# Kernel optimization log

Measured on AMD Instinct MI355X. Metric: run time of the kernel, lower is better.

## Reference

```python
import jax, jax.numpy as jnp
import numpy as np

GROUP_SIZE = 128


def setup_inputs() -> dict:
    key = jax.random.key(0)
    k1, k2, k3 = jax.random.split(key, 3)
    x = (jax.random.normal(k1, (4, 2048, 4096), dtype=jnp.float32)).astype(jnp.float16)
    packed_weight = jax.random.randint(k2, (512, 11008), 0, 2147483647, dtype=jnp.int32)
    scales = jax.random.uniform(k3, (32, 11008), dtype=jnp.float32).astype(jnp.float16)
    return {"x": x, "packed_weight": packed_weight, "scales": scales}


def _dequantize(packed_weight, scales):
    # packed_weight: [K//8, N] int32, 8 nibbles per int32 (nibble i at bits 4i..4i+3)
    # scales: [K//GROUP_SIZE, N]
    Kp, N = packed_weight.shape
    K = Kp * 8
    shifts = (jnp.arange(8, dtype=jnp.int32) * 4)[None, :, None]      # [1,8,1]
    nibbles = (packed_weight[:, None, :] >> shifts) & 15              # [K//8,8,N]
    vals = nibbles.reshape(K, N).astype(jnp.float32)                  # [K,N]
    sc = jnp.repeat(scales.astype(jnp.float32), GROUP_SIZE, axis=0)   # [K,N]
    return (vals - 8.0) / 7.5 * sc


def reference(x, packed_weight, scales):
    K = packed_weight.shape[0] * 8
    N = packed_weight.shape[1]
    deq = _dequantize(packed_weight, scales)                 # [K,N] fp32
    x2 = x.reshape(-1, K).astype(jnp.float32)                # [M,K] fp32 accumulate
    out = jnp.matmul(x2, deq).astype(jnp.float16)            # [M,N] fp16 store
    return out.reshape(*x.shape[:-1], N)
```

## Files before the change

### kernel.cpp

```cpp
#include <hip/hip_runtime.h>
#include <stdint.h>

typedef __attribute__((ext_vector_type(8))) _Float16 half8;
typedef __attribute__((ext_vector_type(2))) _Float16 half2v;
typedef __attribute__((ext_vector_type(4))) float floatx4;
typedef __attribute__((ext_vector_type(4))) uint32_t uint4v;

#define KDIM 4096
#define NDIM 11008
#define NKT 64

#define GLOAD_LDS16(gsrc, ldst)                                                        \
  __builtin_amdgcn_global_load_lds(                                                    \
      (const __attribute__((address_space(1))) void*)(gsrc),                           \
      (__attribute__((address_space(3))) void*)(ldst), 16, 0, 0)

static __device__ __forceinline__ uint32_t pkrtz(float a, float b) {
  auto h = __builtin_amdgcn_cvt_pkrtz(a, b);
  return __builtin_bit_cast(uint32_t, h);
}

static __device__ __forceinline__ half8 dq8(uint32_t q, half2v ssv) {
  half2v off; off[0] = (_Float16)(-1032.0f); off[1] = (_Float16)(-1032.0f);
  const uint32_t a0 = (q & 0x000F000Fu) | 0x64006400u;
  const uint32_t a1 = ((q >> 4) & 0x000F000Fu) | 0x64006400u;
  const uint32_t a2 = ((q >> 8) & 0x000F000Fu) | 0x64006400u;
  const uint32_t a3 = ((q >> 12) & 0x000F000Fu) | 0x64006400u;
  const uint32_t p0 = __builtin_amdgcn_perm(a1, a0, 0x05040100u);
  const uint32_t p1 = __builtin_amdgcn_perm(a3, a2, 0x05040100u);
  const uint32_t p2 = __builtin_amdgcn_perm(a1, a0, 0x07060302u);
  const uint32_t p3 = __builtin_amdgcn_perm(a3, a2, 0x07060302u);
  uint4v u;
  u[0] = __builtin_bit_cast(uint32_t, (__builtin_bit_cast(half2v, p0) + off) * ssv);
  u[1] = __builtin_bit_cast(uint32_t, (__builtin_bit_cast(half2v, p1) + off) * ssv);
  u[2] = __builtin_bit_cast(uint32_t, (__builtin_bit_cast(half2v, p2) + off) * ssv);
  u[3] = __builtin_bit_cast(uint32_t, (__builtin_bit_cast(half2v, p3) + off) * ssv);
  return __builtin_bit_cast(half8, u);
}

__global__ __launch_bounds__(256)
void l4b_prep(const float* __restrict__ in, _Float16* __restrict__ out, int n8) {
  int i = blockIdx.x * 256 + threadIdx.x;
  if (i < n8) {
    floatx4 v0 = ((const floatx4*)in)[2 * i];
    floatx4 v1 = ((const floatx4*)in)[2 * i + 1];
    uint4v u;
    u[0] = pkrtz(v0[0], v0[1]); u[1] = pkrtz(v0[2], v0[3]);
    u[2] = pkrtz(v1[0], v1[1]); u[3] = pkrtz(v1[2], v1[3]);
    ((uint4v*)out)[i] = u;
  }
}

__global__ __launch_bounds__(512, 2)
void l4b_main(const _Float16* __restrict__ XH,
              const int* __restrict__ PW,
              const float* __restrict__ SC,
              float* __restrict__ OUT)
{
  __shared__ alignas(16) _Float16 la[2][256 * 64];
  __shared__ alignas(16) _Float16 lb[2][256 * 64];

  const int tid  = threadIdx.x;
  const int lane = tid & 63;
  const int wave = tid >> 6;

  const int cpx = (int)gridDim.x >> 3;
  const int wg  = ((int)blockIdx.x & 7) * cpx + ((int)blockIdx.x >> 3);
  const int by  = wg / 43;
  const int bx  = wg - by * 43;
  const int64_t brow = (int64_t)by * 256;
  const int     bcol = bx * 256;

  const int wr = (wave >> 2) * 128;
  const int wc = (wave & 3) * 64;
  const int fr = lane & 15;
  const int fq = lane >> 4;

  floatx4 acc[8][4];
#pragma unroll
  for (int i = 0; i < 8; ++i)
#pragma unroll
    for (int j = 0; j < 4; ++j) acc[i][j] = (floatx4)(0.0f);

  const int arow8 = lane >> 3;
  const int aslot = (lane & 7) ^ arow8;
  const _Float16* const asrc0 =
      XH + (brow + wave * 32 + arow8) * (int64_t)KDIM + aslot * 8;

  const int bc  = tid & 255;
  const int bkq = tid >> 8;
  const int*   const pwcol = PW + bcol + bc;
  const float* const sccol = SC + bcol + bc;

  int   rw[4];
  float rsc;

#define DMA_A(t, b)                                                        \
  do {                                                                     \
    _Pragma("unroll") for (int g8 = 0; g8 < 4; ++g8)                       \
        GLOAD_LDS16(asrc0 + (int64_t)g8 * 8 * KDIM + (t) * 64,             \
                    &la[b][(wave * 32 + g8 * 8) * 64]);                    \
  } while (0)

#define LOADB(t)                                                           \
  do {                                                                     \
    const int* pp = pwcol + ((t) * 8 + bkq) * NDIM;                        \
    _Pragma("unroll") for (int j_ = 0; j_ < 4; ++j_)                       \
        rw[j_] = pp[j_ * 2 * NDIM];                                        \
    rsc = sccol[(int64_t)((t) >> 1) * NDIM];                               \
  } while (0)

#define WRITE_B(dst)                                                       \
  do {                                                                     \
    const _Float16 ss = (_Float16)(rsc * (1.0f / 7.5f));                   \
    half2v sv; sv[0] = ss; sv[1] = ss;                                     \
    _Pragma("unroll") for (int j_ = 0; j_ < 4; ++j_) {                     \
      half8 v = dq8((uint32_t)rw[j_], sv);                                 \
      const int kp = bkq + 2 * j_;                                         \
      *(half8*)&(dst)[bc * 64 + ((kp ^ (bc & 7)) * 8)] = v;                \
    }                                                                      \
  } while (0)

#define READ_B4(ksl)                                                       \
  _Pragma("unroll") for (int fn_ = 0; fn_ < 4; ++fn_) {                    \
    const int n_ = wc + fn_ * 16 + fr;                                     \
    bfr[fn_] = *(const half8*)&lbp[n_ * 64 + (((ksl) ^ (n_ & 7)) * 8)];    \
  }

#define READ_A4(fm0, ksl)                                                  \
  _Pragma("unroll") for (int fm_ = 0; fm_ < 4; ++fm_) {                    \
    const int m_ = wr + ((fm0) + fm_) * 16 + fr;                           \
    af[fm_] = *(const half8*)&lap[m_ * 64 + (((ksl) ^ (m_ & 7)) * 8)];     \
  }

#define MFMA16(fm0)                                                        \
  __builtin_amdgcn_s_setprio(1);                                           \
  _Pragma("unroll") for (int fm_ = 0; fm_ < 4; ++fm_)                      \
  _Pragma("unroll") for (int fn_ = 0; fn_ < 4; ++fn_)                      \
      acc[(fm0) + fm_][fn_] = __builtin_amdgcn_mfma_f32_16x16x32_f16(      \
          af[fm_], bfr[fn_], acc[(fm0) + fm_][fn_], 0, 0, 0);              \
  __builtin_amdgcn_s_setprio(0);

#define PH_BAR()                                                           \
  do {                                                                     \
    __builtin_amdgcn_sched_barrier(0);                                     \
    __builtin_amdgcn_s_barrier();                                          \
    __builtin_amdgcn_sched_barrier(0);                                     \
  } while (0)

  LOADB(0);
  DMA_A(0, 0);
  WRITE_B(lb[0]);
  __builtin_amdgcn_sched_barrier(0);
  asm volatile("s_waitcnt vmcnt(0) lgkmcnt(0)" ::: "memory");
  __builtin_amdgcn_s_barrier();
  __builtin_amdgcn_sched_barrier(0);

  for (int kt = 0; kt < NKT; ++kt) {
    const int buf = kt & 1;
    const _Float16* lap = la[buf];
    const _Float16* lbp = lb[buf];
    _Float16* const lbn = lb[buf ^ 1];
    const bool havep = (kt + 1 < NKT);

    half8 af[4], bfr[4];

    READ_B4(fq);
    READ_A4(0, fq);
    if (havep) {
      LOADB(kt + 1);
      DMA_A(kt + 1, buf ^ 1);
    }
    PH_BAR();
    MFMA16(0);
    PH_BAR();

    READ_A4(4, fq);
    PH_BAR();
    MFMA16(4);
    PH_BAR();

    READ_B4(4 + fq);
    READ_A4(0, 4 + fq);
    if (havep) WRITE_B(lbn);
    PH_BAR();
    MFMA16(0);
    PH_BAR();

    READ_A4(4, 4 + fq);
    PH_BAR();
    MFMA16(4);
    __builtin_amdgcn_sched_barrier(0);
    asm volatile("s_waitcnt vmcnt(0) lgkmcnt(0)" ::: "memory");
    __builtin_amdgcn_s_barrier();
    __builtin_amdgcn_sched_barrier(0);
  }

#pragma unroll
  for (int fm = 0; fm < 8; ++fm)
#pragma unroll
    for (int fn = 0; fn < 4; ++fn)
#pragma unroll
      for (int r = 0; r < 4; ++r) {
        const int64_t row = brow + wr + fm * 16 + fq * 4 + r;
        const int     col = bcol + wc + fn * 16 + fr;
        OUT[row * NDIM + col] = acc[fm][fn][r];
      }
}

__global__ __launch_bounds__(512, 2)
void l4b_fb(const float* __restrict__ X, const int* __restrict__ PW,
            const float* __restrict__ SC, float* __restrict__ OUT)
{
  __shared__ alignas(16) _Float16 fla[2][256 * 64];
  __shared__ alignas(16) _Float16 flb[2][256 * 64];

  const int tid  = threadIdx.x;
  const int lane = tid & 63;
  const int wave = tid >> 6;

  const int cpx = (int)gridDim.x >> 3;
  const int wg  = ((int)blockIdx.x & 7) * cpx + ((int)blockIdx.x >> 3);
  const int by  = wg / 43;
  const int bx  = wg - by * 43;
  const int64_t brow = (int64_t)by * 256;
  const int     bcol = bx * 256;

  const int wr = (wave >> 2) * 128;
  const int wc = (wave & 3) * 64;
  const int fr = lane & 15;
  const int fq = lane >> 4;

  floatx4 acc[8][4];
#pragma unroll
  for (int i = 0; i < 8; ++i)
#pragma unroll
    for (int j = 0; j < 4; ++j) acc[i][j] = (floatx4)(0.0f);

  const int ar = tid >> 1;
  const int ah = tid & 1;
  const float* const aptr = X + (brow + ar) * (int64_t)KDIM + ah * 32;
  const int bc  = tid & 255;
  const int bkq = tid >> 8;
  const int*   const pwcol = PW + bcol + bc;
  const float* const sccol = SC + bcol + bc;

  floatx4 ra[8];
  int     rwf[4];
  float   rsc;

#define F_LOAD_A(t)                                                        \
  do {                                                                     \
    const float* ap = aptr + (t) * 64;                                     \
    _Pragma("unroll") for (int i_ = 0; i_ < 8; ++i_)                       \
        ra[i_] = *(const floatx4*)(ap + i_ * 4);                           \
  } while (0)

#define F_LOAD_B(t)                                                        \
  do {                                                                     \
    const int* pp = pwcol + ((t) * 8 + bkq) * NDIM;                        \
    _Pragma("unroll") for (int j_ = 0; j_ < 4; ++j_)                       \
        rwf[j_] = pp[j_ * 2 * NDIM];                                       \
    rsc = sccol[(int64_t)((t) >> 1) * NDIM];                               \
  } while (0)

#define F_WRITE_A(dst)                                                     \
  do {                                                                     \
    _Pragma("unroll") for (int i2 = 0; i2 < 4; ++i2) {                     \
      uint4v u;                                                            \
      u[0] = pkrtz(ra[2 * i2][0], ra[2 * i2][1]);                          \
      u[1] = pkrtz(ra[2 * i2][2], ra[2 * i2][3]);                          \
      u[2] = pkrtz(ra[2 * i2 + 1][0], ra[2 * i2 + 1][1]);                  \
      u[3] = pkrtz(ra[2 * i2 + 1][2], ra[2 * i2 + 1][3]);                  \
      const int s_ = ah * 4 + i2;                                          \
      *(half8*)&(dst)[ar * 64 + ((s_ ^ (ar & 7)) * 8)] =                   \
          __builtin_bit_cast(half8, u);                                    \
    }                                                                      \
  } while (0)

#define F_WRITE_B(dst)                                                     \
  do {                                                                     \
    const _Float16 ssf = (_Float16)(rsc * (1.0f / 7.5f));                  \
    half2v sv; sv[0] = ssf; sv[1] = ssf;                                   \
    _Pragma("unroll") for (int j_ = 0; j_ < 4; ++j_) {                     \
      half8 v = dq8((uint32_t)rwf[j_], sv);                                \
      const int kp = bkq + 2 * j_;                                         \
      *(half8*)&(dst)[bc * 64 + ((kp ^ (bc & 7)) * 8)] = v;                \
    }                                                                      \
  } while (0)

#define F_MFMA16(fm0)                                                      \
  __builtin_amdgcn_s_barrier();                                            \
  asm volatile("s_waitcnt lgkmcnt(0)" ::: "memory");                       \
  __builtin_amdgcn_sched_barrier(0);                                       \
  __builtin_amdgcn_s_setprio(1);                                           \
  _Pragma("unroll") for (int fm_ = 0; fm_ < 4; ++fm_)                      \
  _Pragma("unroll") for (int fn_ = 0; fn_ < 4; ++fn_)                      \
      acc[(fm0) + fm_][fn_] = __builtin_amdgcn_mfma_f32_16x16x32_f16(      \
          af[fm_], bfr[fn_], acc[(fm0) + fm_][fn_], 0, 0, 0);              \
  __builtin_amdgcn_s_setprio(0);                                           \
  __builtin_amdgcn_sched_barrier(0);                                       \
  __builtin_amdgcn_s_barrier();                                            \
  __builtin_amdgcn_sched_barrier(0);

  F_LOAD_A(0); F_LOAD_B(0);
  F_WRITE_A(fla[0]); F_WRITE_B(flb[0]);
  F_LOAD_A(1); F_LOAD_B(1);
  asm volatile("s_waitcnt lgkmcnt(0)" ::: "memory");
  __builtin_amdgcn_s_barrier();
  __builtin_amdgcn_sched_barrier(0);

  for (int kt = 0; kt < NKT; ++kt) {
    const int buf = kt & 1;
    const _Float16* lap = fla[buf];
    const _Float16* lbp = flb[buf];
    _Float16* const lan = fla[buf ^ 1];
    _Float16* const lbn = flb[buf ^ 1];
    const bool haveW = (kt + 1 < NKT);
    const bool haveL = (kt + 2 < NKT);

    half8 bfr[4], af[4];

#pragma unroll
    for (int fn_ = 0; fn_ < 4; ++fn_) {
      const int n_ = wc + fn_ * 16 + fr;
      bfr[fn_] = *(const half8*)&lbp[n_ * 64 + ((fq ^ (n_ & 7)) * 8)];
    }
#pragma unroll
    for (int fm_ = 0; fm_ < 4; ++fm_) {
      const int m_ = wr + fm_ * 16 + fr;
      af[fm_] = *(const half8*)&lap[m_ * 64 + ((fq ^ (m_ & 7)) * 8)];
    }
    if (haveW) F_WRITE_A(lan);
    F_MFMA16(0);

#pragma unroll
    for (int fm_ = 0; fm_ < 4; ++fm_) {
      const int m_ = wr + (4 + fm_) * 16 + fr;
      af[fm_] = *(const half8*)&lap[m_ * 64 + ((fq ^ (m_ & 7)) * 8)];
    }
    if (haveL) F_LOAD_A(kt + 2);
    F_MFMA16(4);

#pragma unroll
    for (int fn_ = 0; fn_ < 4; ++fn_) {
      const int n_ = wc + fn_ * 16 + fr;
      bfr[fn_] = *(const half8*)&lbp[n_ * 64 + (((4 + fq) ^ (n_ & 7)) * 8)];
    }
#pragma unroll
    for (int fm_ = 0; fm_ < 4; ++fm_) {
      const int m_ = wr + fm_ * 16 + fr;
      af[fm_] = *(const half8*)&lap[m_ * 64 + (((4 + fq) ^ (m_ & 7)) * 8)];
    }
    if (haveW) F_WRITE_B(lbn);
    F_MFMA16(0);

#pragma unroll
    for (int fm_ = 0; fm_ < 4; ++fm_) {
      const int m_ = wr + (4 + fm_) * 16 + fr;
      af[fm_] = *(const half8*)&lap[m_ * 64 + (((4 + fq) ^ (m_ & 7)) * 8)];
    }
    if (haveL) F_LOAD_B(kt + 2);
    F_MFMA16(4);
  }

#pragma unroll
  for (int fm = 0; fm < 8; ++fm)
#pragma unroll
    for (int fn = 0; fn < 4; ++fn)
#pragma unroll
      for (int r = 0; r < 4; ++r) {
        const int64_t row = brow + wr + fm * 16 + fq * 4 + r;
        const int     col = bcol + wc + fn * 16 + fr;
        OUT[row * NDIM + col] = acc[fm][fn][r];
      }
}

extern "C" void kernel_launch(void* const* d_in, const int* in_sizes, int n_in,
                              void* d_out, int out_size, void* d_ws, size_t ws_size,
                              hipStream_t stream) {
  const float* X   = (const float*)d_in[0];
  const int*   PW  = (const int*)d_in[1];
  const float* SC  = (const float*)d_in[2];
  float*       OUT = (float*)d_out;

  const int    M     = in_sizes[0] / KDIM;
  const size_t needH = (size_t)in_sizes[0] * 2;
  const int    grid  = (M / 256) * (NDIM / 256);

  if (ws_size >= needH && (M % 256) == 0) {
    _Float16* XH = (_Float16*)d_ws;
    const int n8 = in_sizes[0] / 8;
    l4b_prep<<<(n8 + 255) / 256, 256, 0, stream>>>(X, XH, n8);
    l4b_main<<<grid, 512, 0, stream>>>(XH, PW, SC, OUT);
  } else {
    l4b_fb<<<grid, 512, 0, stream>>>(X, PW, SC, OUT);
  }
}
```

Measured before the change: 850.3 us.

## Deepen global-load pipeline to prefetch two k-tiles ahead with register double-buffering

Restructures the main loop so global loads for A (DMA into LDS) and packed B weights are issued two k-tiles ahead instead of one. B weights go into alternating register sets, and A reuses the just-consumed LDS buffer. It uses partial vmcnt waits so the next tile's loads stay in flight across the barrier. This is meant to hide more global memory latency behind MFMA work, at the cost of extra registers and trickier synchronization.

After: 858.5 us. No clear change (+1.0%).

```diff
diff --git a/kernel.cpp b/kernel.cpp
--- a/kernel.cpp
+++ b/kernel.cpp
@@ -92,45 +92,45 @@
   const int*   const pwcol = PW + bcol + bc;
   const float* const sccol = SC + bcol + bc;
 
-  int   rw[4];
-  float rsc;
-
-#define DMA_A(t, b)                                                        \
+  int   rw0[4], rw1[4];
+  float rs0, rs1;
+
+#define DMA_A(t, dst)                                                      \
   do {                                                                     \
     _Pragma("unroll") for (int g8 = 0; g8 < 4; ++g8)                       \
         GLOAD_LDS16(asrc0 + (int64_t)g8 * 8 * KDIM + (t) * 64,             \
-                    &la[b][(wave * 32 + g8 * 8) * 64]);                    \
-  } while (0)
-
-#define LOADB(t)                                                           \
+                    &(dst)[(wave * 32 + g8 * 8) * 64]);                    \
+  } while (0)
+
+#define LOADB(t, rwv, rs)                                                  \
   do {                                                                     \
     const int* pp = pwcol + ((t) * 8 + bkq) * NDIM;                        \
     _Pragma("unroll") for (int j_ = 0; j_ < 4; ++j_)                       \
-        rw[j_] = pp[j_ * 2 * NDIM];                                        \
-    rsc = sccol[(int64_t)((t) >> 1) * NDIM];                               \
-  } while (0)
-
-#define WRITE_B(dst)                                                       \
-  do {                                                                     \
-    const _Float16 ss = (_Float16)(rsc * (1.0f / 7.5f));                   \
+        rwv[j_] = pp[j_ * 2 * NDIM];                                       \
+    rs = sccol[(int64_t)((t) >> 1) * NDIM];                                \
+  } while (0)
+
+#define WRITE_B(dst, rwv, rs)                                              \
+  do {                                                                     \
+    const _Float16 ss = (_Float16)((rs) * (1.0f / 7.5f));                  \
     half2v sv; sv[0] = ss; sv[1] = ss;                                     \
     _Pragma("unroll") for (int j_ = 0; j_ < 4; ++j_) {                     \
-      half8 v = dq8((uint32_t)rw[j_], sv);                                 \
+      half8 v = dq8((uint32_t)rwv[j_], sv);                                \
       const int kp = bkq + 2 * j_;                                         \
       *(half8*)&(dst)[bc * 64 + ((kp ^ (bc & 7)) * 8)] = v;                \
     }                                                                      \
   } while (0)
 
-#define READ_B4(ksl)                                                       \
+#define READ_B4(src, ksl)                                                  \
   _Pragma("unroll") for (int fn_ = 0; fn_ < 4; ++fn_) {                    \
     const int n_ = wc + fn_ * 16 + fr;                                     \
-    bfr[fn_] = *(const half8*)&lbp[n_ * 64 + (((ksl) ^ (n_ & 7)) * 8)];    \
-  }
-
-#define READ_A4(fm0, ksl)                                                  \
+    bfr[fn_] = *(const half8*)&(src)[n_ * 64 + (((ksl) ^ (n_ & 7)) * 8)];  \
+  }
+
+#define READ_A4(src, fm0, ksl)                                             \
   _Pragma("unroll") for (int fm_ = 0; fm_ < 4; ++fm_) {                    \
     const int m_ = wr + ((fm0) + fm_) * 16 + fr;                           \
-    af[fm_] = *(const half8*)&lap[m_ * 64 + (((ksl) ^ (m_ & 7)) * 8)];     \
+    af[fm_] = *(const half8*)&(src)[m_ * 64 + (((ksl) ^ (m_ & 7)) * 8)];   \
   }
 
 #define MFMA16(fm0)                                                        \
@@ -148,53 +148,64 @@
     __builtin_amdgcn_sched_barrier(0);                                     \
   } while (0)
 
-  LOADB(0);
-  DMA_A(0, 0);
-  WRITE_B(lb[0]);
-  __builtin_amdgcn_sched_barrier(0);
-  asm volatile("s_waitcnt vmcnt(0) lgkmcnt(0)" ::: "memory");
+#define KT_BODY(laP, lbP, lbN, rwc, rsc, rwn, rsn, KT, STG, LDF)           \
+  do {                                                                     \
+    half8 af[4], bfr[4];                                                   \
+                                                                   \
+    READ_B4(lbP, fq);                                                      \
+    READ_A4(laP, 0, fq);                                                   \
+    PH_BAR();                                                              \
+    MFMA16(0);                                                             \
+    PH_BAR();                                                              \
+                                                                   \
+    READ_A4(laP, 4, fq);                                                   \
+    PH_BAR();                                                              \
+    MFMA16(4);                                                             \
+    PH_BAR();                                                              \
+                                                \
+    READ_B4(lbP, 4 + fq);                                                  \
+    READ_A4(laP, 0, 4 + fq);                                               \
+    if (STG) WRITE_B(lbN, rwc, rsc);                                       \
+    PH_BAR();                                                              \
+    MFMA16(0);                                                             \
+    PH_BAR();                                                              \
+        \
+    READ_A4(laP, 4, 4 + fq);                                               \
+    asm volatile("s_waitcnt lgkmcnt(0)" ::: "memory");                     \
+    __builtin_amdgcn_sched_barrier(0);                                     \
+    __builtin_amdgcn_s_barrier();        \
+    __builtin_amdgcn_sched_barrier(0);                                     \
+    if (LDF) {                                                             \
+      LOADB(KT + 2, rwn, rsn);                                 \
+      DMA_A(KT + 2, laP);                                      \
+    }                                                                      \
+    __builtin_amdgcn_sched_barrier(0);                                     \
+    MFMA16(4);                                                             \
+    __builtin_amdgcn_sched_barrier(0);                                     \
+    if (LDF) { asm volatile("s_waitcnt vmcnt(9)" ::: "memory"); }          \
+    else     { asm volatile("s_waitcnt vmcnt(0)" ::: "memory"); }          \
+    __builtin_amdgcn_sched_barrier(0);                                     \
+    __builtin_amdgcn_s_barrier();          \
+    __builtin_amdgcn_sched_barrier(0);                                     \
+  } while (0)
+
+  LOADB(0, rw0, rs0);
+  DMA_A(0, la[0]);
+  WRITE_B(lb[0], rw0, rs0);
+  LOADB(1, rw1, rs1);
+  DMA_A(1, la[1]);
+  asm volatile("s_waitcnt vmcnt(9)" ::: "memory");
+  asm volatile("s_waitcnt lgkmcnt(0)" ::: "memory");
   __builtin_amdgcn_s_barrier();
   __builtin_amdgcn_sched_barrier(0);
 
-  for (int kt = 0; kt < NKT; ++kt) {
-    const int buf = kt & 1;
-    const _Float16* lap = la[buf];
-    const _Float16* lbp = lb[buf];
-    _Float16* const lbn = lb[buf ^ 1];
-    const bool havep = (kt + 1 < NKT);
-
-    half8 af[4], bfr[4];
-
-    READ_B4(fq);
-    READ_A4(0, fq);
-    if (havep) {
-      LOADB(kt + 1);
-      DMA_A(kt + 1, buf ^ 1);
-    }
-    PH_BAR();
-    MFMA16(0);
-    PH_BAR();
-
-    READ_A4(4, fq);
-    PH_BAR();
-    MFMA16(4);
-    PH_BAR();
-
-    READ_B4(4 + fq);
-    READ_A4(0, 4 + fq);
-    if (havep) WRITE_B(lbn);
-    PH_BAR();
-    MFMA16(0);
-    PH_BAR();
-
-    READ_A4(4, 4 + fq);
-    PH_BAR();
-    MFMA16(4);
-    __builtin_amdgcn_sched_barrier(0);
-    asm volatile("s_waitcnt vmcnt(0) lgkmcnt(0)" ::: "memory");
-    __builtin_amdgcn_s_barrier();
-    __builtin_amdgcn_sched_barrier(0);
-  }
+  for (int g = 0; g < 31; ++g) {
+    const int kt = 2 * g;
+    KT_BODY(la[0], lb[0], lb[1], rw1, rs1, rw0, rs0, kt,     true, true);
+    KT_BODY(la[1], lb[1], lb[0], rw0, rs0, rw1, rs1, kt + 1, true, true);
+  }
+  KT_BODY(la[0], lb[0], lb[1], rw1, rs1, rw0, rs0, 62, true,  false);
+  KT_BODY(la[1], lb[1], lb[0], rw0, rs0, rw1, rs1, 63, false, false);
 
 #pragma unroll
   for (int fm = 0; fm < 8; ++fm)
```

## Replace 256x256 tile kernel with 128x128 tile, 256-thread kernel with simpler pipeline

Applied to the files above, without the earlier changes.

The main int4-dequant GEMM kernel moves from 256x256 output tiles with 8 waves to 128x128 tiles with 4 waves, each wave still owning a 64x64 sub-tile. The phased barrier schedule with interleaved LDS reads is replaced by a single phase per k-tile: prefetch, read all fragments, run the MFMAs, then dequantize and write the next B tile. The smaller tiles give more workgroups, but each one reuses loaded data less, so global traffic and B dequantization work rise.

After: 982.9 us. 15.6% more time.

```diff
diff --git a/kernel.cpp b/kernel.cpp
--- a/kernel.cpp
+++ b/kernel.cpp
@@ -51,14 +51,14 @@
   }
 }
 
-__global__ __launch_bounds__(512, 2)
-void l4b_main(const _Float16* __restrict__ XH,
+__global__ __launch_bounds__(256, 2)
+void l4b_g128(const _Float16* __restrict__ XH,
               const int* __restrict__ PW,
               const float* __restrict__ SC,
               float* __restrict__ OUT)
 {
-  __shared__ alignas(16) _Float16 la[2][256 * 64];
-  __shared__ alignas(16) _Float16 lb[2][256 * 64];
+  __shared__ alignas(16) _Float16 la[2][128 * 64];
+  __shared__ alignas(16) _Float16 lb[2][128 * 64];
 
   const int tid  = threadIdx.x;
   const int lane = tid & 63;
@@ -66,19 +66,19 @@
 
   const int cpx = (int)gridDim.x >> 3;
   const int wg  = ((int)blockIdx.x & 7) * cpx + ((int)blockIdx.x >> 3);
-  const int by  = wg / 43;
-  const int bx  = wg - by * 43;
-  const int64_t brow = (int64_t)by * 256;
-  const int     bcol = bx * 256;
-
-  const int wr = (wave >> 2) * 128;
-  const int wc = (wave & 3) * 64;
+  const int by  = wg / 86;
+  const int bx  = wg - by * 86;
+  const int64_t brow = (int64_t)by * 128;
+  const int     bcol = bx * 128;
+
+  const int wr = (wave >> 1) * 64;
+  const int wc = (wave & 1) * 64;
   const int fr = lane & 15;
   const int fq = lane >> 4;
 
-  floatx4 acc[8][4];
-#pragma unroll
-  for (int i = 0; i < 8; ++i)
+  floatx4 acc[4][4];
+#pragma unroll
+  for (int i = 0; i < 4; ++i)
 #pragma unroll
     for (int j = 0; j < 4; ++j) acc[i][j] = (floatx4)(0.0f);
 
@@ -87,32 +87,32 @@
   const _Float16* const asrc0 =
       XH + (brow + wave * 32 + arow8) * (int64_t)KDIM + aslot * 8;
 
-  const int bc  = tid & 255;
-  const int bkq = tid >> 8;
+  const int bc  = tid & 127;
+  const int bkq = tid >> 7;
   const int*   const pwcol = PW + bcol + bc;
   const float* const sccol = SC + bcol + bc;
 
   int   rw[4];
-  float rsc;
-
-#define DMA_A(t, b)                                                        \
+  float rs;
+
+#define G_DMA_A(t, dst)                                                    \
   do {                                                                     \
     _Pragma("unroll") for (int g8 = 0; g8 < 4; ++g8)                       \
         GLOAD_LDS16(asrc0 + (int64_t)g8 * 8 * KDIM + (t) * 64,             \
-                    &la[b][(wave * 32 + g8 * 8) * 64]);                    \
-  } while (0)
-
-#define LOADB(t)                                                           \
+                    &(dst)[(wave * 32 + g8 * 8) * 64]);                    \
+  } while (0)
+
+#define G_LOADB(t)                                                         \
   do {                                                                     \
     const int* pp = pwcol + ((t) * 8 + bkq) * NDIM;                        \
     _Pragma("unroll") for (int j_ = 0; j_ < 4; ++j_)                       \
         rw[j_] = pp[j_ * 2 * NDIM];                                        \
-    rsc = sccol[(int64_t)((t) >> 1) * NDIM];                               \
-  } while (0)
-
-#define WRITE_B(dst)                                                       \
-  do {                                                                     \
-    const _Float16 ss = (_Float16)(rsc * (1.0f / 7.5f));                   \
+    rs = sccol[(int64_t)((t) >> 1) * NDIM];                                \
+  } while (0)
+
+#define G_WRITE_B(dst)                                                     \
+  do {                                                                     \
+    const _Float16 ss = (_Float16)(rs * (1.0f / 7.5f));                    \
     half2v sv; sv[0] = ss; sv[1] = ss;                                     \
     _Pragma("unroll") for (int j_ = 0; j_ < 4; ++j_) {                     \
       half8 v = dq8((uint32_t)rw[j_], sv);                                 \
@@ -121,75 +121,59 @@
     }                                                                      \
   } while (0)
 
-#define READ_B4(ksl)                                                       \
+#define G_READ_A(dstf, ks)                                                 \
+  _Pragma("unroll") for (int fm_ = 0; fm_ < 4; ++fm_) {                    \
+    const int m_ = wr + fm_ * 16 + fr;                                     \
+    dstf[fm_] = *(const half8*)&lap[m_ * 64 + ((((ks)*4 + fq) ^ (m_ & 7)) * 8)]; \
+  }
+
+#define G_READ_B(dstf, ks)                                                 \
   _Pragma("unroll") for (int fn_ = 0; fn_ < 4; ++fn_) {                    \
     const int n_ = wc + fn_ * 16 + fr;                                     \
-    bfr[fn_] = *(const half8*)&lbp[n_ * 64 + (((ksl) ^ (n_ & 7)) * 8)];    \
-  }
-
-#define READ_A4(fm0, ksl)                                                  \
-  _Pragma("unroll") for (int fm_ = 0; fm_ < 4; ++fm_) {                    \
-    const int m_ = wr + ((fm0) + fm_) * 16 + fr;                           \
-    af[fm_] = *(const half8*)&lap[m_ * 64 + (((ksl) ^ (m_ & 7)) * 8)];     \
-  }
-
-#define MFMA16(fm0)                                                        \
-  __builtin_amdgcn_s_setprio(1);                                           \
-  _Pragma("unroll") for (int fm_ = 0; fm_ < 4; ++fm_)                      \
-  _Pragma("unroll") for (int fn_ = 0; fn_ < 4; ++fn_)                      \
-      acc[(fm0) + fm_][fn_] = __builtin_amdgcn_mfma_f32_16x16x32_f16(      \
-          af[fm_], bfr[fn_], acc[(fm0) + fm_][fn_], 0, 0, 0);              \
-  __builtin_amdgcn_s_setprio(0);
-
-#define PH_BAR()                                                           \
-  do {                                                                     \
-    __builtin_amdgcn_sched_barrier(0);                                     \
-    __builtin_amdgcn_s_barrier();                                          \
-    __builtin_amdgcn_sched_barrier(0);                                     \
-  } while (0)
-
-  LOADB(0);
-  DMA_A(0, 0);
-  WRITE_B(lb[0]);
-  __builtin_amdgcn_sched_barrier(0);
+    dstf[fn_] = *(const half8*)&lbp[n_ * 64 + ((((ks)*4 + fq) ^ (n_ & 7)) * 8)]; \
+  }
+
+  G_LOADB(0);
+  G_DMA_A(0, la[0]);
+  G_WRITE_B(lb[0]);
   asm volatile("s_waitcnt vmcnt(0) lgkmcnt(0)" ::: "memory");
   __builtin_amdgcn_s_barrier();
   __builtin_amdgcn_sched_barrier(0);
 
   for (int kt = 0; kt < NKT; ++kt) {
-    const int buf = kt & 1;
-    const _Float16* lap = la[buf];
-    const _Float16* lbp = lb[buf];
-    _Float16* const lbn = lb[buf ^ 1];
+    const _Float16* lap = la[kt & 1];
+    const _Float16* lbp = lb[kt & 1];
+    _Float16* const lan = la[(kt & 1) ^ 1];
+    _Float16* const lbn = lb[(kt & 1) ^ 1];
     const bool havep = (kt + 1 < NKT);
 
-    half8 af[4], bfr[4];
-
-    READ_B4(fq);
-    READ_A4(0, fq);
     if (havep) {
-      LOADB(kt + 1);
-      DMA_A(kt + 1, buf ^ 1);
-    }
-    PH_BAR();
-    MFMA16(0);
-    PH_BAR();
-
-    READ_A4(4, fq);
-    PH_BAR();
-    MFMA16(4);
-    PH_BAR();
-
-    READ_B4(4 + fq);
-    READ_A4(0, 4 + fq);
-    if (havep) WRITE_B(lbn);
-    PH_BAR();
-    MFMA16(0);
-    PH_BAR();
-
-    READ_A4(4, 4 + fq);
-    PH_BAR();
-    MFMA16(4);
+      G_LOADB(kt + 1);
+      G_DMA_A(kt + 1, lan);
+    }
+    __builtin_amdgcn_sched_barrier(0);
+
+    half8 af0[4], bf0[4], af1[4], bf1[4];
+    G_READ_A(af0, 0); G_READ_B(bf0, 0);
+    G_READ_A(af1, 1); G_READ_B(bf1, 1);
+
+    __builtin_amdgcn_s_setprio(1);
+#pragma unroll
+    for (int fm_ = 0; fm_ < 4; ++fm_)
+#pragma unroll
+      for (int fn_ = 0; fn_ < 4; ++fn_)
+        acc[fm_][fn_] = __builtin_amdgcn_mfma_f32_16x16x32_f16(
+            af0[fm_], bf0[fn_], acc[fm_][fn_], 0, 0, 0);
+#pragma unroll
+    for (int fm_ = 0; fm_ < 4; ++fm_)
+#pragma unroll
+      for (int fn_ = 0; fn_ < 4; ++fn_)
+        acc[fm_][fn_] = __builtin_amdgcn_mfma_f32_16x16x32_f16(
+            af1[fm_], bf1[fn_], acc[fm_][fn_], 0, 0, 0);
+    __builtin_amdgcn_s_setprio(0);
+
+    if (havep) G_WRITE_B(lbn);
+
     __builtin_amdgcn_sched_barrier(0);
     asm volatile("s_waitcnt vmcnt(0) lgkmcnt(0)" ::: "memory");
     __builtin_amdgcn_s_barrier();
@@ -197,7 +181,7 @@
   }
 
 #pragma unroll
-  for (int fm = 0; fm < 8; ++fm)
+  for (int fm = 0; fm < 4; ++fm)
 #pragma unroll
     for (int fn = 0; fn < 4; ++fn)
 #pragma unroll
@@ -386,14 +370,15 @@
 
   const int    M     = in_sizes[0] / KDIM;
   const size_t needH = (size_t)in_sizes[0] * 2;
-  const int    grid  = (M / 256) * (NDIM / 256);
-
-  if (ws_size >= needH && (M % 256) == 0) {
+
+  if (ws_size >= needH && (M % 128) == 0) {
     _Float16* XH = (_Float16*)d_ws;
     const int n8 = in_sizes[0] / 8;
     l4b_prep<<<(n8 + 255) / 256, 256, 0, stream>>>(X, XH, n8);
-    l4b_main<<<grid, 512, 0, stream>>>(XH, PW, SC, OUT);
+    const int grid = (M / 128) * (NDIM / 128);
+    l4b_g128<<<grid, 256, 0, stream>>>(XH, PW, SC, OUT);
   } else {
+    const int grid = (M / 256) * (NDIM / 256);
     l4b_fb<<<grid, 512, 0, stream>>>(X, PW, SC, OUT);
   }
 }
```

## Pre-dequantize weights to fp16 transposed buffer and DMA both operands to LDS

Applied to the files above, without the earlier changes.

Adds a prep kernel that dequantizes the packed int4 weights once per call into an fp16 [N,K] workspace buffer. The GEMM then loads both A and B straight into LDS with global_load_lds, removing per-tile register dequantization and the VALU work inside the main loop. The cost is an extra ~90MB write and read of fp16 weights per call. The existing main kernel's barrier placement is also reshuffled. The new path runs only when the workspace is large enough.

Measured after the change: 872.1 us. +2.6%, slower.

```diff
diff --git a/kernel.cpp b/kernel.cpp
--- a/kernel.cpp
+++ b/kernel.cpp
@@ -51,6 +51,171 @@
   }
 }
 
+__global__ __launch_bounds__(256)
+void l4b_prepB(const int* __restrict__ PW, const float* __restrict__ SC,
+               _Float16* __restrict__ BH) {
+  __shared__ alignas(16) _Float16 lt[64 * 64];
+  const int t  = threadIdx.x;
+  const int nb = NDIM / 64;
+  const int kb = blockIdx.x / nb;
+  const int n0 = (blockIdx.x - kb * nb) * 64;
+  const int kp0 = kb * 8;
+#pragma unroll
+  for (int h = 0; h < 2; ++h) {
+    const int idx  = t + h * 256;
+    const int kp_l = idx >> 6;
+    const int n_l  = idx & 63;
+    const int kp   = kp0 + kp_l;
+    const uint32_t q = (uint32_t)PW[kp * NDIM + n0 + n_l];
+    const float    s = SC[(kp >> 4) * NDIM + n0 + n_l];
+    const _Float16 ss = (_Float16)(s * (1.0f / 7.5f));
+    half2v sv; sv[0] = ss; sv[1] = ss;
+    half8 v = dq8(q, sv);
+    *(half8*)&lt[n_l * 64 + ((kp_l ^ (n_l & 7)) * 8)] = v;
+  }
+  __syncthreads();
+  const int n_l = t >> 2;
+  const int c   = t & 3;
+  uint4v o0 = *(uint4v*)&lt[n_l * 64 + (((c * 2) ^ (n_l & 7)) * 8)];
+  uint4v o1 = *(uint4v*)&lt[n_l * 64 + (((c * 2 + 1) ^ (n_l & 7)) * 8)];
+  _Float16* op = BH + (int64_t)(n0 + n_l) * KDIM + kp0 * 8 + c * 16;
+  *(uint4v*)op       = o0;
+  *(uint4v*)(op + 8) = o1;
+}
+
+__global__ __launch_bounds__(512, 2)
+void l4b_g2(const _Float16* __restrict__ XH,
+            const _Float16* __restrict__ BH,
+            float* __restrict__ OUT)
+{
+  __shared__ alignas(16) _Float16 la[2][256 * 64];
+  __shared__ alignas(16) _Float16 lb[2][256 * 64];
+
+  const int tid  = threadIdx.x;
+  const int lane = tid & 63;
+  const int wave = tid >> 6;
+
+  const int cpx = (int)gridDim.x >> 3;
+  const int wg  = ((int)blockIdx.x & 7) * cpx + ((int)blockIdx.x >> 3);
+  const int by  = wg / 43;
+  const int bx  = wg - by * 43;
+  const int64_t brow = (int64_t)by * 256;
+  const int     bcol = bx * 256;
+
+  const int wr = (wave >> 2) * 128;
+  const int wc = (wave & 3) * 64;
+  const int fr = lane & 15;
+  const int fq = lane >> 4;
+
+  floatx4 acc[8][4];
+#pragma unroll
+  for (int i = 0; i < 8; ++i)
+#pragma unroll
+    for (int j = 0; j < 4; ++j) acc[i][j] = (floatx4)(0.0f);
+
+  const int arow8 = lane >> 3;
+  const int aslot = (lane & 7) ^ arow8;
+  const _Float16* const asrc0 =
+      XH + (brow + wave * 32 + arow8) * (int64_t)KDIM + aslot * 8;
+  const _Float16* const bsrc0 =
+      BH + (bcol + wave * 32 + arow8) * (int64_t)KDIM + aslot * 8;
+
+#define DMA1(srcb, t, dst, g8)                                             \
+  GLOAD_LDS16((srcb) + (int64_t)(g8) * 8 * KDIM + (t) * 64,                \
+              &(dst)[(wave * 32 + (g8) * 8) * 64])
+
+#define READ_B4(src, ksl)                                                  \
+  _Pragma("unroll") for (int fn_ = 0; fn_ < 4; ++fn_) {                    \
+    const int n_ = wc + fn_ * 16 + fr;                                     \
+    bfr[fn_] = *(const half8*)&(src)[n_ * 64 + (((ksl) ^ (n_ & 7)) * 8)];  \
+  }
+
+#define READ_A4(src, fm0, ksl)                                             \
+  _Pragma("unroll") for (int fm_ = 0; fm_ < 4; ++fm_) {                    \
+    const int m_ = wr + ((fm0) + fm_) * 16 + fr;                           \
+    af[fm_] = *(const half8*)&(src)[m_ * 64 + (((ksl) ^ (m_ & 7)) * 8)];   \
+  }
+
+#define MFMA16(fm0)                                                        \
+  _Pragma("unroll") for (int fm_ = 0; fm_ < 4; ++fm_)                      \
+  _Pragma("unroll") for (int fn_ = 0; fn_ < 4; ++fn_)                      \
+      acc[(fm0) + fm_][fn_] = __builtin_amdgcn_mfma_f32_16x16x32_f16(      \
+          af[fm_], bfr[fn_], acc[(fm0) + fm_][fn_], 0, 0, 0);
+
+#define PHASE_MFMA(fm0)                                                    \
+  __builtin_amdgcn_sched_barrier(0);                                       \
+  __builtin_amdgcn_s_barrier();                                            \
+  asm volatile("s_waitcnt lgkmcnt(0)" ::: "memory");                       \
+  __builtin_amdgcn_sched_barrier(0);                                       \
+  __builtin_amdgcn_s_setprio(1);                                           \
+  MFMA16(fm0);                                                             \
+  __builtin_amdgcn_s_setprio(0);                                           \
+  __builtin_amdgcn_sched_barrier(0);                                       \
+  __builtin_amdgcn_s_barrier();                                            \
+  __builtin_amdgcn_sched_barrier(0);
+
+#pragma unroll
+  for (int g8 = 0; g8 < 4; ++g8) DMA1(asrc0, 0, la[0], g8);
+#pragma unroll
+  for (int g8 = 0; g8 < 4; ++g8) DMA1(bsrc0, 0, lb[0], g8);
+  asm volatile("s_waitcnt vmcnt(0) lgkmcnt(0)" ::: "memory");
+  __builtin_amdgcn_s_barrier();
+  __builtin_amdgcn_sched_barrier(0);
+
+  for (int kt = 0; kt < NKT; ++kt) {
+    const _Float16* lap = la[kt & 1];
+    const _Float16* lbp = lb[kt & 1];
+    _Float16* const lan = la[(kt & 1) ^ 1];
+    _Float16* const lbn = lb[(kt & 1) ^ 1];
+    const bool havep = (kt + 1 < NKT);
+
+    half8 af[4], bfr[4];
+
+    READ_B4(lbp, fq);
+    READ_A4(lap, 0, fq);
+    if (havep) {
+      DMA1(asrc0, kt + 1, lan, 0); DMA1(asrc0, kt + 1, lan, 1);
+      DMA1(bsrc0, kt + 1, lbn, 0); DMA1(bsrc0, kt + 1, lbn, 1);
+    }
+    PHASE_MFMA(0);
+
+    READ_A4(lap, 4, fq);
+    if (havep) {
+      DMA1(asrc0, kt + 1, lan, 2); DMA1(asrc0, kt + 1, lan, 3);
+      DMA1(bsrc0, kt + 1, lbn, 2); DMA1(bsrc0, kt + 1, lbn, 3);
+    }
+    PHASE_MFMA(4);
+
+    READ_B4(lbp, 4 + fq);
+    READ_A4(lap, 0, 4 + fq);
+    PHASE_MFMA(0);
+
+    READ_A4(lap, 4, 4 + fq);
+    __builtin_amdgcn_sched_barrier(0);
+    __builtin_amdgcn_s_barrier();
+    asm volatile("s_waitcnt lgkmcnt(0)" ::: "memory");
+    __builtin_amdgcn_sched_barrier(0);
+    __builtin_amdgcn_s_setprio(1);
+    MFMA16(4);
+    __builtin_amdgcn_s_setprio(0);
+    __builtin_amdgcn_sched_barrier(0);
+    asm volatile("s_waitcnt vmcnt(0)" ::: "memory");
+    __builtin_amdgcn_s_barrier();
+    __builtin_amdgcn_sched_barrier(0);
+  }
+
+#pragma unroll
+  for (int fm = 0; fm < 8; ++fm)
+#pragma unroll
+    for (int fn = 0; fn < 4; ++fn)
+#pragma unroll
+      for (int r = 0; r < 4; ++r) {
+        const int64_t row = brow + wr + fm * 16 + fq * 4 + r;
+        const int     col = bcol + wc + fn * 16 + fr;
+        OUT[row * NDIM + col] = acc[fm][fn][r];
+      }
+}
+
 __global__ __launch_bounds__(512, 2)
 void l4b_main(const _Float16* __restrict__ XH,
               const int* __restrict__ PW,
@@ -95,14 +260,14 @@
   int   rw[4];
   float rsc;
 
-#define DMA_A(t, b)                                                        \
+#define M_DMA_A(t, dst)                                                    \
   do {                                                                     \
     _Pragma("unroll") for (int g8 = 0; g8 < 4; ++g8)                       \
         GLOAD_LDS16(asrc0 + (int64_t)g8 * 8 * KDIM + (t) * 64,             \
-                    &la[b][(wave * 32 + g8 * 8) * 64]);                    \
-  } while (0)
-
-#define LOADB(t)                                                           \
+                    &(dst)[(wave * 32 + g8 * 8) * 64]);                    \
+  } while (0)
+
+#define M_LOADB(t)                                                         \
   do {                                                                     \
     const int* pp = pwcol + ((t) * 8 + bkq) * NDIM;                        \
     _Pragma("unroll") for (int j_ = 0; j_ < 4; ++j_)                       \
@@ -110,7 +275,7 @@
     rsc = sccol[(int64_t)((t) >> 1) * NDIM];                               \
   } while (0)
 
-#define WRITE_B(dst)                                                       \
+#define M_WRITE_B(dst)                                                     \
   do {                                                                     \
     const _Float16 ss = (_Float16)(rsc * (1.0f / 7.5f));                   \
     half2v sv; sv[0] = ss; sv[1] = ss;                                     \
@@ -121,36 +286,35 @@
     }                                                                      \
   } while (0)
 
-#define READ_B4(ksl)                                                       \
+#define M_READ_B4(ksl)                                                     \
   _Pragma("unroll") for (int fn_ = 0; fn_ < 4; ++fn_) {                    \
     const int n_ = wc + fn_ * 16 + fr;                                     \
     bfr[fn_] = *(const half8*)&lbp[n_ * 64 + (((ksl) ^ (n_ & 7)) * 8)];    \
   }
 
-#define READ_A4(fm0, ksl)                                                  \
+#define M_READ_A4(fm0, ksl)                                                \
   _Pragma("unroll") for (int fm_ = 0; fm_ < 4; ++fm_) {                    \
     const int m_ = wr + ((fm0) + fm_) * 16 + fr;                           \
     af[fm_] = *(const half8*)&lap[m_ * 64 + (((ksl) ^ (m_ & 7)) * 8)];     \
   }
 
-#define MFMA16(fm0)                                                        \
+#define M_MFMA16(fm0)                                                      \
+  __builtin_amdgcn_s_barrier();                                            \
+  asm volatile("s_waitcnt lgkmcnt(0)" ::: "memory");                       \
+  __builtin_amdgcn_sched_barrier(0);                                       \
   __builtin_amdgcn_s_setprio(1);                                           \
   _Pragma("unroll") for (int fm_ = 0; fm_ < 4; ++fm_)                      \
   _Pragma("unroll") for (int fn_ = 0; fn_ < 4; ++fn_)                      \
       acc[(fm0) + fm_][fn_] = __builtin_amdgcn_mfma_f32_16x16x32_f16(      \
           af[fm_], bfr[fn_], acc[(fm0) + fm_][fn_], 0, 0, 0);              \
-  __builtin_amdgcn_s_setprio(0);
-
-#define PH_BAR()                                                           \
-  do {                                                                     \
-    __builtin_amdgcn_sched_barrier(0);                                     \
-    __builtin_amdgcn_s_barrier();                                          \
-    __builtin_amdgcn_sched_barrier(0);                                     \
-  } while (0)
-
-  LOADB(0);
-  DMA_A(0, 0);
-  WRITE_B(lb[0]);
+  __builtin_amdgcn_s_setprio(0);                                           \
+  __builtin_amdgcn_sched_barrier(0);                                       \
+  __builtin_amdgcn_s_barrier();                                            \
+  __builtin_amdgcn_sched_barrier(0);
+
+  M_LOADB(0);
+  M_DMA_A(0, la[0]);
+  M_WRITE_B(lb[0]);
   __builtin_amdgcn_sched_barrier(0);
   asm volatile("s_waitcnt vmcnt(0) lgkmcnt(0)" ::: "memory");
   __builtin_amdgcn_s_barrier();
@@ -160,36 +324,37 @@
     const int buf = kt & 1;
     const _Float16* lap = la[buf];
     const _Float16* lbp = lb[buf];
+    _Float16* const lan = la[buf ^ 1];
     _Float16* const lbn = lb[buf ^ 1];
     const bool havep = (kt + 1 < NKT);
 
     half8 af[4], bfr[4];
 
-    READ_B4(fq);
-    READ_A4(0, fq);
-    if (havep) {
-      LOADB(kt + 1);
-      DMA_A(kt + 1, buf ^ 1);
-    }
-    PH_BAR();
-    MFMA16(0);
-    PH_BAR();
-
-    READ_A4(4, fq);
-    PH_BAR();
-    MFMA16(4);
-    PH_BAR();
-
-    READ_B4(4 + fq);
-    READ_A4(0, 4 + fq);
-    if (havep) WRITE_B(lbn);
-    PH_BAR();
-    MFMA16(0);
-    PH_BAR();
-
-    READ_A4(4, 4 + fq);
-    PH_BAR();
-    MFMA16(4);
+    M_READ_B4(fq);
+    M_READ_A4(0, fq);
+    if (havep) { M_LOADB(kt + 1); M_DMA_A(kt + 1, lan); }
+    M_MFMA16(0);
+
+    M_READ_A4(4, fq);
+    M_MFMA16(4);
+
+    M_READ_B4(4 + fq);
+    M_READ_A4(0, 4 + fq);
+    if (havep) M_WRITE_B(lbn);
+    M_MFMA16(0);
+
+    M_READ_A4(4, 4 + fq);
+    __builtin_amdgcn_s_barrier();
+    asm volatile("s_waitcnt lgkmcnt(0)" ::: "memory");
+    __builtin_amdgcn_sched_barrier(0);
+    __builtin_amdgcn_s_setprio(1);
+#pragma unroll
+    for (int fm_ = 0; fm_ < 4; ++fm_)
+#pragma unroll
+      for (int fn_ = 0; fn_ < 4; ++fn_)
+        acc[4 + fm_][fn_] = __builtin_amdgcn_mfma_f32_16x16x32_f16(
+            af[fm_], bfr[fn_], acc[4 + fm_][fn_], 0, 0, 0);
+    __builtin_amdgcn_s_setprio(0);
     __builtin_amdgcn_sched_barrier(0);
     asm volatile("s_waitcnt vmcnt(0) lgkmcnt(0)" ::: "memory");
     __builtin_amdgcn_s_barrier();
@@ -386,9 +551,17 @@
 
   const int    M     = in_sizes[0] / KDIM;
   const size_t needH = (size_t)in_sizes[0] * 2;
+  const size_t needB = (size_t)KDIM * NDIM * 2;
   const int    grid  = (M / 256) * (NDIM / 256);
 
-  if (ws_size >= needH && (M % 256) == 0) {
+  if (ws_size >= needH + needB && (M % 256) == 0) {
+    _Float16* XH = (_Float16*)d_ws;
+    _Float16* BH = (_Float16*)((char*)d_ws + needH);
+    const int n8 = in_sizes[0] / 8;
+    l4b_prep<<<(n8 + 255) / 256, 256, 0, stream>>>(X, XH, n8);
+    l4b_prepB<<<(KDIM / 64) * (NDIM / 64), 256, 0, stream>>>(PW, SC, BH);
+    l4b_g2<<<grid, 512, 0, stream>>>(XH, BH, OUT);
+  } else if (ws_size >= needH && (M % 256) == 0) {
     _Float16* XH = (_Float16*)d_ws;
     const int n8 = in_sizes[0] / 8;
     l4b_prep<<<(n8 + 255) / 256, 256, 0, stream>>>(X, XH, n8);
```
